# Optimization experiments

Measured on AMD Instinct MI355X. Metric: run time of the kernel, lower is better.

## Reference

```python
import jax, jax.numpy as jnp
import numpy as np

EPS = 1e-5  # torch BatchNorm1d default eps


def _bn(x, p):
    # eval-mode batchnorm; p = stacked [gamma, beta, running_mean, running_var], shape [4, C]
    g, b, m, v = p
    return (x - m[:, None]) * jax.lax.rsqrt(v[:, None] + EPS) * g[:, None] + b[:, None]


def _conv(w, x):
    # 1x1 Conv1d == channel matmul: w [O,C], x [B,C,N] -> [B,O,N]
    return jnp.einsum('oc,bcn->bon', w, x)


def _sa(x, qk_w, v_w, v_b, t_w, t_b, bnp):
    # offset self-attention; q_conv.weight is tied to k_conv.weight in the original
    q = jnp.einsum('oc,bcn->bno', qk_w, x)          # [B,N,C/4]
    k = _conv(qk_w, x)                              # [B,C/4,N]
    v = _conv(v_w, x) + v_b[None, :, None]          # [B,C,N]
    attn = jax.nn.softmax(jnp.einsum('bno,bom->bnm', q, k), axis=-1)  # [B,N,N]
    attn = attn / (1e-9 + attn.sum(axis=1, keepdims=True))            # L1 re-norm over dim 1
    x_r = jnp.einsum('bcn,bnm->bcm', v, attn)       # [B,C,N]
    x_r = jax.nn.relu(_bn(_conv(t_w, x - x_r) + t_b[None, :, None], bnp))
    return x + x_r


def setup_inputs():
    key = jax.random.key(0)
    ks = iter(jax.random.split(key, 64))
    def n(shape, s=0.1):
        return jax.random.normal(next(ks), shape, jnp.float32) * s
    def bn_p(c):
        g = jax.random.uniform(next(ks), (c,), jnp.float32, 0.5, 1.5)
        b = n((c,))
        m = n((c,))
        v = jax.random.uniform(next(ks), (c,), jnp.float32, 0.5, 1.5)
        return jnp.stack([g, b, m, v])
    B, C, N = 16, 16, 2048
    return {
        'x': jax.random.normal(next(ks), (B, C, N), jnp.float32),
        'conv1_w': n((128, 16)), 'bn1': bn_p(128),
        'conv2_w': n((16, 128)), 'bn2': bn_p(16),
        'sa_qk_w': n((4, 4, 16)), 'sa_v_w': n((4, 16, 16)), 'sa_v_b': n((4, 16)),
        'sa_trans_w': n((4, 16, 16)), 'sa_trans_b': n((4, 16)),
        'sa_bn': jnp.stack([bn_p(16) for _ in range(4)]),
        'fuse_w': n((128, 64)), 'fuse_bn': bn_p(128),
        'convs1_w': n((512, 264)), 'convs1_b': n((512,)), 'bns1': bn_p(512),
        'convs2_w': n((256, 512)), 'convs2_b': n((256,)), 'bns2': bn_p(256),
        'convs3_w': n((16, 256)), 'convs3_b': n((16,)),
    }


def reference(x, conv1_w, bn1, conv2_w, bn2, sa_qk_w, sa_v_w, sa_v_b,
              sa_trans_w, sa_trans_b, sa_bn, fuse_w, fuse_bn,
              convs1_w, convs1_b, bns1, convs2_w, convs2_b, bns2,
              convs3_w, convs3_b):
    B, _, N = x.shape
    h = jax.nn.relu(_bn(_conv(conv1_w, x), bn1))   # [B,128,N]
    h = jax.nn.relu(_bn(_conv(conv2_w, h), bn2))   # [B,16,N]
    feats = []
    for i in range(4):
        h = _sa(h, sa_qk_w[i], sa_v_w[i], sa_v_b[i], sa_trans_w[i], sa_trans_b[i], sa_bn[i])
        feats.append(h)
    xqq = jnp.concatenate(feats, axis=1)           # [B,64,N]
    xqqw = jax.nn.leaky_relu(_bn(_conv(fuse_w, xqq), fuse_bn), 0.2)  # [B,128,N]
    # faithful to original (including the [1]-indexing quirk):
    x_max = jnp.argmax(xqqw, axis=2)               # [B,128] argmax indices (torch.max(...)[1])
    x_avg = jnp.mean(xqqw, axis=2)[1]              # [128] batch element 1's channel means
    x_max_f = jnp.broadcast_to(x_max.astype(jnp.float32)[:, :, None], (B, 128, N))
    x_avg_f = jnp.broadcast_to(x_avg.reshape(B, -1)[:, :, None], (B, 128 // B, N))
    g = jnp.concatenate([xqqw, x_max_f, x_avg_f], axis=1)  # [B,264,N]
    g = jax.nn.relu(_bn(_conv(convs1_w, g) + convs1_b[None, :, None], bns1))
    # dropout is identity in eval mode
    g = jax.nn.relu(_bn(_conv(convs2_w, g) + convs2_b[None, :, None], bns2))
    return _conv(convs3_w, g) + convs3_b[None, :, None]  # [B,16,N]
```

## Files before the change

### kernel.cpp

```cpp
#include <hip/hip_runtime.h>
#include <stdint.h>

typedef __bf16 bf16_t;
typedef __bf16 bf16x8 __attribute__((ext_vector_type(8)));
typedef __bf16 bf16x4 __attribute__((ext_vector_type(4)));
typedef float f32x4 __attribute__((ext_vector_type(4)));
typedef float f32x2 __attribute__((ext_vector_type(2)));

#define LOG2E 1.4426950408889634f

__device__ __forceinline__ float relu_(float v) { return v > 0.f ? v : 0.f; }

__global__ __launch_bounds__(256) void k_prep(
    const float* __restrict__ convs1_w, const float* __restrict__ convs2_w,
    const float* __restrict__ bn1, const float* __restrict__ bn2,
    const float* __restrict__ sa_bn, const float* __restrict__ sa_trans_b,
    const float* __restrict__ fuse_bn, const float* __restrict__ convs1_b,
    const float* __restrict__ bns1, const float* __restrict__ convs2_b,
    const float* __restrict__ bns2,
    bf16_t* __restrict__ wbuf1, bf16_t* __restrict__ wbuf2, float* __restrict__ params)
{
  int idx = blockIdx.x * 256 + threadIdx.x;
  for (int it = 0; it < 3; ++it) {
    int i = idx + it * 65536;
    if (i < 65536) {
      int o = i >> 7, c = i & 127;
      wbuf1[i] = (bf16_t)convs1_w[o * 264 + c];
    } else if (i < 65536 + 131072) {
      int j = i - 65536;
      wbuf2[j] = (bf16_t)convs2_w[j];
    }
  }
  if (blockIdx.x == 0) {
    for (int t = threadIdx.x; t < 1104; t += 256) {
      float g, be, m, v, extra = 0.f; int so, ho;
      if (t < 128)      { g=bn1[t]; be=bn1[128+t]; m=bn1[256+t]; v=bn1[384+t]; so=t; ho=128+t; }
      else if (t < 144) { int u=t-128; g=bn2[u]; be=bn2[16+u]; m=bn2[32+u]; v=bn2[48+u]; so=256+u; ho=272+u; }
      else if (t < 208) { int u=t-144; int L=u>>4, o=u&15; const float* p=sa_bn+L*64;
                          g=p[o]; be=p[16+o]; m=p[32+o]; v=p[48+o];
                          extra=sa_trans_b[L*16+o]; so=288+u; ho=352+u; }
      else if (t < 336) { int u=t-208; g=fuse_bn[u]; be=fuse_bn[128+u]; m=fuse_bn[256+u]; v=fuse_bn[384+u]; so=416+u; ho=544+u; }
      else if (t < 848) { int u=t-336; g=bns1[u]; be=bns1[512+u]; m=bns1[1024+u]; v=bns1[1536+u]; extra=convs1_b[u]; so=672+u; ho=1184+u; }
      else              { int u=t-848; g=bns2[u]; be=bns2[256+u]; m=bns2[512+u]; v=bns2[768+u]; extra=convs2_b[u]; so=1696+u; ho=1952+u; }
      float sc = g * rsqrtf(v + 1e-5f);
      params[so] = sc;
      params[ho] = (extra - m) * sc + be;
    }
  }
}

__global__ __launch_bounds__(256) void k_convs(const float* __restrict__ x,
    const float* __restrict__ w1, const float* __restrict__ w2,
    const float* __restrict__ params, const float* __restrict__ qk_w,
    const float* __restrict__ v_w, const float* __restrict__ v_b,
    float* __restrict__ h0, float* __restrict__ kbuf, float* __restrict__ vbufT)
{
  __shared__ float xs[16 * 64];
  __shared__ float ws1[128 * 17];
  __shared__ float ws2[16 * 129];
  __shared__ __align__(16) float h1s[128 * 64];
  __shared__ float hcv[64 * 17];
  __shared__ float qk[64], vw[256], vb[16], sc1[128], sh1[128], sc2[16], sh2[16];
  int t = threadIdx.x;
  int bid = blockIdx.x;
  int b = bid >> 5, n0 = (bid & 31) * 64;
  for (int i = t; i < 1024; i += 256) { int c = i >> 6, col = i & 63; xs[i] = x[((size_t)b * 16 + c) * 2048 + n0 + col]; }
  for (int i = t; i < 2048; i += 256) { int o = i >> 4, c = i & 15;  ws1[o * 17 + c]  = w1[i]; }
  for (int i = t; i < 2048; i += 256) { int o = i >> 7, c = i & 127; ws2[o * 129 + c] = w2[i]; }
  if (t < 64) qk[t] = qk_w[t];
  vw[t] = v_w[t];
  if (t < 16) { vb[t] = v_b[t]; sc2[t] = params[256 + t]; sh2[t] = params[272 + t]; }
  if (t < 128) { sc1[t] = params[t]; sh1[t] = params[128 + t]; }
  __syncthreads();
  int col = t & 63, og = t >> 6;
  float xr[16];
#pragma unroll
  for (int c = 0; c < 16; ++c) xr[c] = xs[c * 64 + col];
#pragma unroll 4
  for (int i = 0; i < 32; ++i) {
    int o = og * 32 + i;
    float s = 0.f;
#pragma unroll
    for (int c = 0; c < 16; ++c) s = fmaf(ws1[o * 17 + c], xr[c], s);
    h1s[o * 64 + col] = relu_(fmaf(s, sc1[o], sh1[o]));
  }
  __syncthreads();
  float a[4] = {0.f, 0.f, 0.f, 0.f};
  for (int c = 0; c < 128; ++c) {
    float hv = h1s[c * 64 + col];
#pragma unroll
    for (int oo = 0; oo < 4; ++oo) a[oo] = fmaf(ws2[(og * 4 + oo) * 129 + c], hv, a[oo]);
  }
#pragma unroll
  for (int oo = 0; oo < 4; ++oo) {
    int o = og * 4 + oo;
    float v = relu_(fmaf(a[oo], sc2[o], sh2[o]));
    h0[((size_t)b * 16 + o) * 2048 + n0 + col] = v;
    hcv[col * 17 + o] = v;
  }
  __syncthreads();
  float hr[16];
#pragma unroll
  for (int c = 0; c < 16; ++c) hr[c] = hcv[col * 17 + c];
#pragma unroll
  for (int i = 0; i < 5; ++i) {
    int u = og * 5 + i;
    const float* W = (u < 4) ? &qk[u * 16] : &vw[(u - 4) * 16];
    float s = (u < 4) ? 0.f : vb[u - 4];
#pragma unroll
    for (int c = 0; c < 16; ++c) s = fmaf(W[c], hr[c], s);
    if (u < 4) kbuf[((size_t)b * 2048 + n0 + col) * 4 + u] = s;
    else       vbufT[((size_t)b * 2048 + n0 + col) * 16 + (u - 4)] = s;
  }
}

__global__ __launch_bounds__(256) void k_rowstats(const float* __restrict__ kbuf, float* __restrict__ Lpart)
{
  __shared__ float4 kch[128];
  int bid = blockIdx.x;
  int b = bid >> 7, nt = (bid >> 4) & 7, ms = bid & 15;
  int t = threadIdx.x;
  const float4* kb = (const float4*)kbuf + b * 2048;
  if (t < 128) kch[t] = kb[ms * 128 + t];
  __syncthreads();
  int n = nt * 256 + t;
  float4 q = kb[n];
  q.x *= LOG2E; q.y *= LOG2E; q.z *= LOG2E; q.w *= LOG2E;
  float L = 0.f;
#pragma unroll 4
  for (int m = 0; m < 128; ++m) {
    float4 k4 = kch[m];
    float s = fmaf(q.x, k4.x, fmaf(q.y, k4.y, fmaf(q.z, k4.z, q.w * k4.w)));
    L += exp2f(s);
  }
  Lpart[((size_t)ms * 16 + b) * 2048 + n] = L;
}

__global__ __launch_bounds__(256) void k_colaccum(const float* __restrict__ kbuf, const float* __restrict__ vbufT,
    const float* __restrict__ Lpart, float* __restrict__ parts)
{
  __shared__ __align__(16) float ku[128 * 8];
  __shared__ __align__(16) float vch[128 * 16];
  int bid = blockIdx.x;
  int b = bid >> 6, mt = (bid >> 4) & 3, ns = bid & 15;
  int t = threadIdx.x;
  if (t < 128) {
    int n = ns * 128 + t;
    float4 k4 = ((const float4*)kbuf)[b * 2048 + n];
    float Ls = 0.f;
#pragma unroll
    for (int s = 0; s < 16; ++s) Ls += Lpart[((size_t)s * 16 + b) * 2048 + n];
    *(float4*)&ku[t * 8] = k4;
    ku[t * 8 + 4] = -__log2f(Ls);
  } else {
    int s = t - 128;
    int n = ns * 128 + s;
    const float4* vp = (const float4*)&vbufT[((size_t)b * 2048 + n) * 16];
    *(float4*)&vch[s * 16 + 0]  = vp[0];
    *(float4*)&vch[s * 16 + 4]  = vp[1];
    *(float4*)&vch[s * 16 + 8]  = vp[2];
    *(float4*)&vch[s * 16 + 12] = vp[3];
  }
  __syncthreads();
  int m0 = mt * 512 + t;
  float4 qa = ((const float4*)kbuf)[b * 2048 + m0];
  float4 qb = ((const float4*)kbuf)[b * 2048 + m0 + 256];
  qa.x *= LOG2E; qa.y *= LOG2E; qa.z *= LOG2E; qa.w *= LOG2E;
  qb.x *= LOG2E; qb.y *= LOG2E; qb.z *= LOG2E; qb.w *= LOG2E;
  f32x2 acc0[8], acc1[8];
#pragma unroll
  for (int j = 0; j < 8; ++j) { acc0[j] = (f32x2){0.f, 0.f}; acc1[j] = (f32x2){0.f, 0.f}; }
  float den0 = 0.f, den1 = 0.f;
#pragma unroll 2
  for (int nn = 0; nn < 128; ++nn) {
    f32x4 k4 = *(const f32x4*)&ku[nn * 8];
    float lg = ku[nn * 8 + 4];
    float s0 = fmaf(qa.x, k4[0], fmaf(qa.y, k4[1], fmaf(qa.z, k4[2], fmaf(qa.w, k4[3], lg))));
    float s1 = fmaf(qb.x, k4[0], fmaf(qb.y, k4[1], fmaf(qb.z, k4[2], fmaf(qb.w, k4[3], lg))));
    float e0 = exp2f(s0), e1 = exp2f(s1);
    den0 += e0; den1 += e1;
    f32x4 va = *(const f32x4*)&vch[nn * 16 + 0];
    f32x4 vbb = *(const f32x4*)&vch[nn * 16 + 4];
    f32x4 vc = *(const f32x4*)&vch[nn * 16 + 8];
    f32x4 vd = *(const f32x4*)&vch[nn * 16 + 12];
    f32x2 ev0 = {e0, e0}, ev1 = {e1, e1};
    f32x2 p0 = {va[0], va[1]},  p1 = {va[2], va[3]};
    f32x2 p2 = {vbb[0], vbb[1]}, p3 = {vbb[2], vbb[3]};
    f32x2 p4 = {vc[0], vc[1]},  p5 = {vc[2], vc[3]};
    f32x2 p6 = {vd[0], vd[1]},  p7 = {vd[2], vd[3]};
    acc0[0] += ev0 * p0; acc0[1] += ev0 * p1; acc0[2] += ev0 * p2; acc0[3] += ev0 * p3;
    acc0[4] += ev0 * p4; acc0[5] += ev0 * p5; acc0[6] += ev0 * p6; acc0[7] += ev0 * p7;
    acc1[0] += ev1 * p0; acc1[1] += ev1 * p1; acc1[2] += ev1 * p2; acc1[3] += ev1 * p3;
    acc1[4] += ev1 * p4; acc1[5] += ev1 * p5; acc1[6] += ev1 * p6; acc1[7] += ev1 * p7;
  }
  float* p = parts + ((size_t)(ns * 16 + b) * 17) * 2048 + m0;
#pragma unroll
  for (int c = 0; c < 16; ++c) p[(size_t)c * 2048] = acc0[c >> 1][c & 1];
  p[(size_t)16 * 2048] = den0;
  p += 256;
#pragma unroll
  for (int c = 0; c < 16; ++c) p[(size_t)c * 2048] = acc1[c >> 1][c & 1];
  p[(size_t)16 * 2048] = den1;
}

__global__ __launch_bounds__(256) void k_epilogue(const float* __restrict__ parts,
    const float* __restrict__ hin, int hbs, const float* __restrict__ t_w,
    const float* __restrict__ params, int layer, float* __restrict__ hout,
    const float* __restrict__ qk_w, const float* __restrict__ v_w, const float* __restrict__ v_b,
    float* __restrict__ kbuf, float* __restrict__ vbufT)
{
  __shared__ __align__(16) float pd[17 * 64];
  __shared__ float hs[16 * 64];
  __shared__ float dl[16 * 64];
  __shared__ float hv[64 * 17];
  __shared__ float tw[256], qk[64], vw[256], vb[16], sc[16], sh[16];
  int t = threadIdx.x;
  int bid = blockIdx.x;
  int b = bid >> 5, n0 = (bid & 31) * 64;
  tw[t] = t_w[t];
  if (qk_w) { if (t < 64) qk[t] = qk_w[t]; vw[t] = v_w[t]; if (t < 16) vb[t] = v_b[t]; }
  if (t < 16) { sc[t] = params[288 + layer * 16 + t]; sh[t] = params[352 + layer * 16 + t]; }
  for (int i = t; i < 272; i += 256) {
    int r = i >> 4, c4 = (i & 15) << 2;
    f32x4 s = {0.f, 0.f, 0.f, 0.f};
#pragma unroll
    for (int sp = 0; sp < 16; ++sp)
      s += *(const f32x4*)&parts[((size_t)(sp * 16 + b) * 17 + r) * 2048 + n0 + c4];
    *(f32x4*)&pd[r * 64 + c4] = s;
  }
  for (int i = t; i < 1024; i += 256) {
    int c = i >> 6, col = i & 63;
    hs[i] = hin[(size_t)b * hbs + (size_t)c * 2048 + n0 + col];
  }
  __syncthreads();
  int col = t & 63, g4 = t >> 6;
  float inv = 1.f / (1e-9f + pd[16 * 64 + col]);
#pragma unroll
  for (int j = 0; j < 4; ++j) {
    int c = g4 * 4 + j;
    dl[c * 64 + col] = hs[c * 64 + col] - pd[c * 64 + col] * inv;
  }
  __syncthreads();
#pragma unroll
  for (int j = 0; j < 4; ++j) {
    int o = g4 * 4 + j;
    float y = 0.f;
#pragma unroll
    for (int c = 0; c < 16; ++c) y = fmaf(tw[o * 16 + c], dl[c * 64 + col], y);
    y = relu_(fmaf(y, sc[o], sh[o]));
    float hh = hs[o * 64 + col] + y;
    hout[(size_t)b * 64 * 2048 + (size_t)o * 2048 + n0 + col] = hh;
    hv[col * 17 + o] = hh;
  }
  if (qk_w) {
    __syncthreads();
    float hr[16];
#pragma unroll
    for (int c = 0; c < 16; ++c) hr[c] = hv[col * 17 + c];
#pragma unroll
    for (int i = 0; i < 5; ++i) {
      int u = g4 * 5 + i;
      const float* W = (u < 4) ? &qk[u * 16] : &vw[(u - 4) * 16];
      float s = (u < 4) ? 0.f : vb[u - 4];
#pragma unroll
      for (int c = 0; c < 16; ++c) s = fmaf(W[c], hr[c], s);
      if (u < 4) kbuf[((size_t)b * 2048 + n0 + col) * 4 + u] = s;
      else       vbufT[((size_t)b * 2048 + n0 + col) * 16 + (u - 4)] = s;
    }
  }
}

__global__ __launch_bounds__(256) void k_fuse(const float* __restrict__ feats, const float* __restrict__ fw,
    const float* __restrict__ params, float* __restrict__ xqqw, bf16_t* __restrict__ gbuf)
{
  __shared__ float ws[128 * 65];
  __shared__ __align__(16) float fst[64 * 64];
  __shared__ float sc[128], sh[128];
  int t = threadIdx.x, bid = blockIdx.x;
  int b = bid >> 5, n0 = (bid & 31) * 64;
  for (int i = t; i < 8192; i += 256) { int o = i >> 6, c = i & 63; ws[o * 65 + c] = fw[i]; }
  for (int i = t; i < 4096; i += 256) { int c = i >> 6, col = i & 63; fst[i] = feats[((size_t)b * 64 + c) * 2048 + n0 + col]; }
  if (t < 128) { sc[t] = params[416 + t]; sh[t] = params[544 + t]; }
  __syncthreads();
  int cg = t & 7, og = t >> 3;
  f32x2 acc[4][4];
#pragma unroll
  for (int oo = 0; oo < 4; ++oo)
#pragma unroll
    for (int j = 0; j < 4; ++j) acc[oo][j] = (f32x2){0.f, 0.f};
  for (int c = 0; c < 64; ++c) {
    const f32x2* fp = (const f32x2*)&fst[c * 64 + cg * 8];
    f32x2 f0 = fp[0], f1 = fp[1], f2v = fp[2], f3 = fp[3];
#pragma unroll
    for (int oo = 0; oo < 4; ++oo) {
      float w = ws[(og * 4 + oo) * 65 + c];
      f32x2 wv = {w, w};
      acc[oo][0] += wv * f0; acc[oo][1] += wv * f1;
      acc[oo][2] += wv * f2v; acc[oo][3] += wv * f3;
    }
  }
  float y[4][8];
#pragma unroll
  for (int oo = 0; oo < 4; ++oo) {
    int o = og * 4 + oo;
    float s0 = sc[o], s1 = sh[o];
#pragma unroll
    for (int j = 0; j < 8; ++j) {
      float v = fmaf(acc[oo][j >> 1][j & 1], s0, s1);
      y[oo][j] = v > 0.f ? v : 0.2f * v;
    }
    float4 v0 = {y[oo][0], y[oo][1], y[oo][2], y[oo][3]};
    float4 v1 = {y[oo][4], y[oo][5], y[oo][6], y[oo][7]};
    *(float4*)&xqqw[((size_t)b * 128 + o) * 2048 + n0 + cg * 8] = v0;
    *(float4*)&xqqw[((size_t)b * 128 + o) * 2048 + n0 + cg * 8 + 4] = v1;
  }
#pragma unroll
  for (int j = 0; j < 8; ++j) {
    int col = n0 + cg * 8 + j;
    bf16x4 pk;
    pk[0] = (bf16_t)y[0][j]; pk[1] = (bf16_t)y[1][j];
    pk[2] = (bf16_t)y[2][j]; pk[3] = (bf16_t)y[3][j];
    *(bf16x4*)&gbuf[((size_t)b * 2048 + col) * 128 + og * 4] = pk;
  }
}

__global__ __launch_bounds__(256) void k_argmax(const float* __restrict__ xqqw,
    float* __restrict__ xmaxf, float* __restrict__ xavg)
{
  __shared__ float sv[256]; __shared__ int si[256]; __shared__ float ss[256];
  int bo = blockIdx.x;
  int b = bo >> 7, o = bo & 127;
  const float* row = xqqw + (size_t)bo * 2048;
  int tid = threadIdx.x;
  float best = -3.4e38f; int bi = 0; float sum = 0.f;
#pragma unroll
  for (int j = 0; j < 8; ++j) {
    int n = j * 256 + tid;
    float v = row[n];
    sum += v;
    if (v > best) { best = v; bi = n; }
  }
  sv[tid] = best; si[tid] = bi; ss[tid] = sum;
  __syncthreads();
  for (int s = 128; s > 0; s >>= 1) {
    if (tid < s) {
      float v2 = sv[tid + s]; int i2 = si[tid + s];
      if (v2 > sv[tid] || (v2 == sv[tid] && i2 < si[tid])) { sv[tid] = v2; si[tid] = i2; }
      ss[tid] += ss[tid + s];
    }
    __syncthreads();
  }
  if (tid == 0) {
    xmaxf[bo] = (float)si[0];
    if (b == 1) xavg[o] = ss[0] * (1.0f / 2048.0f);
  }
}

__global__ __launch_bounds__(256) void k_bias2(const float* __restrict__ w1,
    const float* __restrict__ xmaxf, const float* __restrict__ xavg,
    const float* __restrict__ params, float* __restrict__ bias2)
{
  int id = blockIdx.x * 256 + threadIdx.x;
  int o = id >> 4, b = id & 15;
  const float* wr = w1 + (size_t)o * 264;
  float s = 0.f;
  for (int u = 0; u < 128; ++u) s = fmaf(wr[128 + u], xmaxf[b * 128 + u], s);
#pragma unroll
  for (int u = 0; u < 8; ++u)  s = fmaf(wr[256 + u], xavg[b * 8 + u], s);
  bias2[b * 512 + o] = s * params[672 + o];
}

__global__ __launch_bounds__(256) void k_gemm(const bf16_t* __restrict__ A, const bf16_t* __restrict__ Bm,
    const float* __restrict__ scp, const float* __restrict__ shp, const float* __restrict__ bias2,
    bf16_t* __restrict__ Cout, int M, int K, int mtiles)
{
  __shared__ bf16_t At[128 * 32];
  __shared__ bf16_t Bt[128 * 32];
  int tid = threadIdx.x;
  int mt = blockIdx.x % mtiles, ct = blockIdx.x / mtiles;
  int srow = tid >> 2, scol = (tid & 3) << 3;
  const bf16_t* ga = A  + (size_t)(mt * 128 + srow) * K + scol;
  const bf16_t* gb = Bm + (size_t)(ct * 128 + srow) * K + scol;
  int lane = tid & 63, wave = tid >> 6;
  int wr = (wave >> 1) * 64, wc = (wave & 1) * 64;
  int frow = lane & 15, fk = (lane >> 4) * 8;
  const f32x4 z4 = {0.f, 0.f, 0.f, 0.f};
  f32x4 acc[4][4];
#pragma unroll
  for (int i = 0; i < 4; ++i)
#pragma unroll
    for (int j = 0; j < 4; ++j) acc[i][j] = z4;
  uint4 ra0 = *(const uint4*)ga, ra1 = *(const uint4*)(ga + (size_t)64 * K);
  uint4 rb0 = *(const uint4*)gb, rb1 = *(const uint4*)(gb + (size_t)64 * K);
  int ksteps = K >> 5;
  for (int ks = 0; ks < ksteps; ++ks) {
    __syncthreads();
    *(uint4*)&At[tid * 8] = ra0;  *(uint4*)&At[2048 + tid * 8] = ra1;
    *(uint4*)&Bt[tid * 8] = rb0;  *(uint4*)&Bt[2048 + tid * 8] = rb1;
    __syncthreads();
    if (ks + 1 < ksteps) {
      ra0 = *(const uint4*)(ga + (ks + 1) * 32);
      ra1 = *(const uint4*)(ga + (size_t)64 * K + (ks + 1) * 32);
      rb0 = *(const uint4*)(gb + (ks + 1) * 32);
      rb1 = *(const uint4*)(gb + (size_t)64 * K + (ks + 1) * 32);
    }
    bf16x8 af[4], bfr[4];
#pragma unroll
    for (int i = 0; i < 4; ++i) af[i]  = *(const bf16x8*)&At[(wr + i * 16 + frow) * 32 + fk];
#pragma unroll
    for (int j = 0; j < 4; ++j) bfr[j] = *(const bf16x8*)&Bt[(wc + j * 16 + frow) * 32 + fk];
#pragma unroll
    for (int i = 0; i < 4; ++i)
#pragma unroll
      for (int j = 0; j < 4; ++j)
        acc[i][j] = __builtin_amdgcn_mfma_f32_16x16x32_bf16(af[i], bfr[j], acc[i][j], 0, 0, 0);
  }
  int crow = (lane >> 4) * 4, ccol = lane & 15;
#pragma unroll
  for (int i = 0; i < 4; ++i) {
    int o0 = mt * 128 + wr + i * 16 + crow;
    float s0 = scp[o0], s1 = scp[o0+1], s2 = scp[o0+2], s3 = scp[o0+3];
    float t0 = shp[o0], t1 = shp[o0+1], t2 = shp[o0+2], t3 = shp[o0+3];
#pragma unroll
    for (int j = 0; j < 4; ++j) {
      int bn = ct * 128 + wc + j * 16 + ccol;
      float b0 = 0.f, b1 = 0.f, b2 = 0.f, b3 = 0.f;
      if (bias2) {
        const float* bp = bias2 + (size_t)(bn >> 11) * M + o0;
        b0 = bp[0]; b1 = bp[1]; b2 = bp[2]; b3 = bp[3];
      }
      bf16x4 pk;
      pk[0] = (bf16_t)relu_(fmaf(acc[i][j][0], s0, t0 + b0));
      pk[1] = (bf16_t)relu_(fmaf(acc[i][j][1], s1, t1 + b1));
      pk[2] = (bf16_t)relu_(fmaf(acc[i][j][2], s2, t2 + b2));
      pk[3] = (bf16_t)relu_(fmaf(acc[i][j][3], s3, t3 + b3));
      *(bf16x4*)(Cout + (size_t)bn * M + o0) = pk;
    }
  }
}

__global__ __launch_bounds__(256) void k_gemm3(const bf16_t* __restrict__ g2, const float* __restrict__ w3,
    const float* __restrict__ b3, float* __restrict__ out)
{
  __shared__ float wsT[4096];
  __shared__ float bb[16];
  int t = threadIdx.x;
  for (int i = t; i < 4096; i += 256) { int o = i >> 8, k = i & 255; wsT[k * 16 + o] = w3[i]; }
  if (t < 16) bb[t] = b3[t];
  __syncthreads();
  int col = blockIdx.x * 64 + (t & 63);
  int og = t >> 6;
  int b = col >> 11, n = col & 2047;
  const bf16_t* g = g2 + (size_t)col * 256;
  float acc[4] = {0.f, 0.f, 0.f, 0.f};
  for (int k0 = 0; k0 < 256; k0 += 8) {
    bf16x8 gv8 = *(const bf16x8*)(g + k0);
#pragma unroll
    for (int kk = 0; kk < 8; ++kk) {
      float gv = (float)gv8[kk];
      const float* wr = &wsT[(k0 + kk) * 16 + og * 4];
#pragma unroll
      for (int oo = 0; oo < 4; ++oo) acc[oo] = fmaf(wr[oo], gv, acc[oo]);
    }
  }
  float* op = out + (size_t)b * 16 * 2048 + n;
#pragma unroll
  for (int oo = 0; oo < 4; ++oo) {
    int o = og * 4 + oo;
    op[(size_t)o * 2048] = acc[oo] + bb[o];
  }
}

extern "C" void kernel_launch(void* const* d_in, const int* in_sizes, int n_in,
                              void* d_out, int out_size, void* d_ws, size_t ws_size,
                              hipStream_t stream)
{
  const float* x         = (const float*)d_in[0];
  const float* conv1_w   = (const float*)d_in[1];
  const float* bn1       = (const float*)d_in[2];
  const float* conv2_w   = (const float*)d_in[3];
  const float* bn2       = (const float*)d_in[4];
  const float* sa_qk_w   = (const float*)d_in[5];
  const float* sa_v_w    = (const float*)d_in[6];
  const float* sa_v_b    = (const float*)d_in[7];
  const float* sa_trans_w= (const float*)d_in[8];
  const float* sa_trans_b= (const float*)d_in[9];
  const float* sa_bn     = (const float*)d_in[10];
  const float* fuse_w    = (const float*)d_in[11];
  const float* fuse_bn   = (const float*)d_in[12];
  const float* convs1_w  = (const float*)d_in[13];
  const float* convs1_b  = (const float*)d_in[14];
  const float* bns1      = (const float*)d_in[15];
  const float* convs2_w  = (const float*)d_in[16];
  const float* convs2_b  = (const float*)d_in[17];
  const float* bns2      = (const float*)d_in[18];
  const float* convs3_w  = (const float*)d_in[19];
  const float* convs3_b  = (const float*)d_in[20];

  char* ws = (char*)d_ws;
  float*  xqqw  = (float*)(ws + 0);
  float*  feats = (float*)(ws + 16777216);
  float*  h0    = (float*)(ws + 25165824);
  float*  kbuf  = (float*)(ws + 27262976);
  float*  vbufT = (float*)(ws + 27787264);
  float*  Lpart = (float*)(ws + 29884416);
  float*  parts = (float*)(ws + 31981568);
  bf16_t* g1    = (bf16_t*)(ws + 0);
  bf16_t* g2    = (bf16_t*)(ws + 33554432);
  bf16_t* gbuf  = (bf16_t*)(ws + 50331648);
  bf16_t* wbuf1 = (bf16_t*)(ws + 67633152);
  bf16_t* wbuf2 = (bf16_t*)(ws + 67764224);
  float*  params= (float*)(ws + 68026368);
  float*  xmaxf = (float*)(ws + 68042752);
  float*  xavg  = (float*)(ws + 68050944);
  float*  bias2 = (float*)(ws + 68055040);

  k_prep<<<256, 256, 0, stream>>>(convs1_w, convs2_w, bn1, bn2, sa_bn, sa_trans_b, fuse_bn,
                                  convs1_b, bns1, convs2_b, bns2, wbuf1, wbuf2, params);
  k_convs<<<512, 256, 0, stream>>>(x, conv1_w, conv2_w, params, sa_qk_w, sa_v_w, sa_v_b,
                                   h0, kbuf, vbufT);
  for (int i = 0; i < 4; ++i) {
    k_rowstats<<<2048, 256, 0, stream>>>(kbuf, Lpart);
    k_colaccum<<<1024, 256, 0, stream>>>(kbuf, vbufT, Lpart, parts);
    const float* hin = (i == 0) ? h0 : (feats + (size_t)(i - 1) * 16 * 2048);
    int hbs = (i == 0) ? 16 * 2048 : 64 * 2048;
    bool last = (i == 3);
    k_epilogue<<<512, 256, 0, stream>>>(parts, hin, hbs, sa_trans_w + i * 256, params, i,
        feats + (size_t)i * 16 * 2048,
        last ? nullptr : sa_qk_w + (i + 1) * 64,
        last ? nullptr : sa_v_w + (i + 1) * 256,
        last ? nullptr : sa_v_b + (i + 1) * 16,
        kbuf, vbufT);
  }
  k_fuse<<<512, 256, 0, stream>>>(feats, fuse_w, params, xqqw, gbuf);
  k_argmax<<<2048, 256, 0, stream>>>(xqqw, xmaxf, xavg);
  k_bias2<<<32, 256, 0, stream>>>(convs1_w, xmaxf, xavg, params, bias2);
  k_gemm<<<1024, 256, 0, stream>>>(wbuf1, gbuf, params + 672, params + 1184, bias2, g1, 512, 128, 4);
  k_gemm<<<512, 256, 0, stream>>>(wbuf2, g1, params + 1696, params + 1952, nullptr, g2, 256, 512, 2);
  k_gemm3<<<512, 256, 0, stream>>>(g2, convs3_w, convs3_b, (float*)d_out);
}
```

Before: 518.3 us.

## Move attention column accumulation to bf16 MFMA with split-precision and atomic row sums

The scalar FMA loop that accumulated exp-weighted V columns and denominators is replaced by a kernel that issues 16x16x32 bf16 MFMA instructions. Both V and the exponentials are split into hi/lo bf16 parts so the products keep close to fp32 accuracy, and a ones-vector MFMA produces the column sums. Row-stat partial sums are now combined with atomicAdd into a per-layer buffer that the prep kernel zeroes, which removes the 16-way partial read in the consumer. The cost is three MFMAs per product plus extra conversion work, and atomic float adds make the summation order nondeterministic.

```diff
diff --git a/kernel.cpp b/kernel.cpp
--- a/kernel.cpp
+++ b/kernel.cpp
@@ -18,9 +18,12 @@
     const float* __restrict__ fuse_bn, const float* __restrict__ convs1_b,
     const float* __restrict__ bns1, const float* __restrict__ convs2_b,
     const float* __restrict__ bns2,
-    bf16_t* __restrict__ wbuf1, bf16_t* __restrict__ wbuf2, float* __restrict__ params)
+    bf16_t* __restrict__ wbuf1, bf16_t* __restrict__ wbuf2, float* __restrict__ params,
+    float* __restrict__ Lbuf)
 {
   int idx = blockIdx.x * 256 + threadIdx.x;
+  Lbuf[idx] = 0.f;
+  Lbuf[idx + 65536] = 0.f;
   for (int it = 0; it < 3; ++it) {
     int i = idx + it * 65536;
     if (i < 65536) {
@@ -114,7 +117,7 @@
   }
 }
 
-__global__ __launch_bounds__(256) void k_rowstats(const float* __restrict__ kbuf, float* __restrict__ Lpart)
+__global__ __launch_bounds__(256) void k_rowstats(const float* __restrict__ kbuf, float* __restrict__ Lb)
 {
   __shared__ float4 kch[128];
   int bid = blockIdx.x;
@@ -133,74 +136,80 @@
     float s = fmaf(q.x, k4.x, fmaf(q.y, k4.y, fmaf(q.z, k4.z, q.w * k4.w)));
     L += exp2f(s);
   }
-  Lpart[((size_t)ms * 16 + b) * 2048 + n] = L;
-}
-
-__global__ __launch_bounds__(256) void k_colaccum(const float* __restrict__ kbuf, const float* __restrict__ vbufT,
-    const float* __restrict__ Lpart, float* __restrict__ parts)
-{
-  __shared__ __align__(16) float ku[128 * 8];
-  __shared__ __align__(16) float vch[128 * 16];
+  atomicAdd(&Lb[b * 2048 + n], L);
+}
+
+__global__ __launch_bounds__(256, 4) void k_attn(const float* __restrict__ kbuf,
+    const float* __restrict__ vbufT, const float* __restrict__ Lb, float* __restrict__ parts)
+{
+  __shared__ float skn[128 * 8];
+  __shared__ __align__(16) float4 skm[512];
+  int t = threadIdx.x;
   int bid = blockIdx.x;
-  int b = bid >> 6, mt = (bid >> 4) & 3, ns = bid & 15;
-  int t = threadIdx.x;
+  int b = bid >> 6, ns = (bid >> 2) & 15, mq = bid & 3;
   if (t < 128) {
     int n = ns * 128 + t;
     float4 k4 = ((const float4*)kbuf)[b * 2048 + n];
-    float Ls = 0.f;
-#pragma unroll
-    for (int s = 0; s < 16; ++s) Ls += Lpart[((size_t)s * 16 + b) * 2048 + n];
-    *(float4*)&ku[t * 8] = k4;
-    ku[t * 8 + 4] = -__log2f(Ls);
-  } else {
-    int s = t - 128;
-    int n = ns * 128 + s;
-    const float4* vp = (const float4*)&vbufT[((size_t)b * 2048 + n) * 16];
-    *(float4*)&vch[s * 16 + 0]  = vp[0];
-    *(float4*)&vch[s * 16 + 4]  = vp[1];
-    *(float4*)&vch[s * 16 + 8]  = vp[2];
-    *(float4*)&vch[s * 16 + 12] = vp[3];
-  }
-  __syncthreads();
-  int m0 = mt * 512 + t;
-  float4 qa = ((const float4*)kbuf)[b * 2048 + m0];
-  float4 qb = ((const float4*)kbuf)[b * 2048 + m0 + 256];
-  qa.x *= LOG2E; qa.y *= LOG2E; qa.z *= LOG2E; qa.w *= LOG2E;
-  qb.x *= LOG2E; qb.y *= LOG2E; qb.z *= LOG2E; qb.w *= LOG2E;
-  f32x2 acc0[8], acc1[8];
-#pragma unroll
-  for (int j = 0; j < 8; ++j) { acc0[j] = (f32x2){0.f, 0.f}; acc1[j] = (f32x2){0.f, 0.f}; }
-  float den0 = 0.f, den1 = 0.f;
-#pragma unroll 2
-  for (int nn = 0; nn < 128; ++nn) {
-    f32x4 k4 = *(const f32x4*)&ku[nn * 8];
-    float lg = ku[nn * 8 + 4];
-    float s0 = fmaf(qa.x, k4[0], fmaf(qa.y, k4[1], fmaf(qa.z, k4[2], fmaf(qa.w, k4[3], lg))));
-    float s1 = fmaf(qb.x, k4[0], fmaf(qb.y, k4[1], fmaf(qb.z, k4[2], fmaf(qb.w, k4[3], lg))));
-    float e0 = exp2f(s0), e1 = exp2f(s1);
-    den0 += e0; den1 += e1;
-    f32x4 va = *(const f32x4*)&vch[nn * 16 + 0];
-    f32x4 vbb = *(const f32x4*)&vch[nn * 16 + 4];
-    f32x4 vc = *(const f32x4*)&vch[nn * 16 + 8];
-    f32x4 vd = *(const f32x4*)&vch[nn * 16 + 12];
-    f32x2 ev0 = {e0, e0}, ev1 = {e1, e1};
-    f32x2 p0 = {va[0], va[1]},  p1 = {va[2], va[3]};
-    f32x2 p2 = {vbb[0], vbb[1]}, p3 = {vbb[2], vbb[3]};
-    f32x2 p4 = {vc[0], vc[1]},  p5 = {vc[2], vc[3]};
-    f32x2 p6 = {vd[0], vd[1]},  p7 = {vd[2], vd[3]};
-    acc0[0] += ev0 * p0; acc0[1] += ev0 * p1; acc0[2] += ev0 * p2; acc0[3] += ev0 * p3;
-    acc0[4] += ev0 * p4; acc0[5] += ev0 * p5; acc0[6] += ev0 * p6; acc0[7] += ev0 * p7;
-    acc1[0] += ev1 * p0; acc1[1] += ev1 * p1; acc1[2] += ev1 * p2; acc1[3] += ev1 * p3;
-    acc1[4] += ev1 * p4; acc1[5] += ev1 * p5; acc1[6] += ev1 * p6; acc1[7] += ev1 * p7;
-  }
-  float* p = parts + ((size_t)(ns * 16 + b) * 17) * 2048 + m0;
-#pragma unroll
-  for (int c = 0; c < 16; ++c) p[(size_t)c * 2048] = acc0[c >> 1][c & 1];
-  p[(size_t)16 * 2048] = den0;
-  p += 256;
-#pragma unroll
-  for (int c = 0; c < 16; ++c) p[(size_t)c * 2048] = acc1[c >> 1][c & 1];
-  p[(size_t)16 * 2048] = den1;
+    *(float4*)&skn[t * 8] = k4;
+    skn[t * 8 + 4] = -__log2f(Lb[b * 2048 + n]);
+  }
+  skm[t]       = ((const float4*)kbuf)[b * 2048 + mq * 512 + t];
+  skm[t + 256] = ((const float4*)kbuf)[b * 2048 + mq * 512 + t + 256];
+  __syncthreads();
+  int lane = t & 63, w = t >> 6;
+  int lg16 = lane >> 4, c = lane & 15;
+  bf16x8 vhi[4], vlo[4];
+#pragma unroll
+  for (int s = 0; s < 4; ++s) {
+#pragma unroll
+    for (int j = 0; j < 8; ++j) {
+      int n = ns * 128 + s * 32 + lg16 * 8 + j;
+      float v = vbufT[((size_t)b * 2048 + n) * 16 + c];
+      bf16_t h = (bf16_t)v;
+      vhi[s][j] = h;
+      vlo[s][j] = (bf16_t)(v - (float)h);
+    }
+  }
+  bf16x8 ones;
+#pragma unroll
+  for (int j = 0; j < 8; ++j) ones[j] = (bf16_t)1.0f;
+
+  float* pb = parts + ((size_t)(ns * 16 + b) * 17) * 2048;
+  for (int it = 0; it < 8; ++it) {
+    int tm = w * 8 + it;
+    int mb = mq * 512 + tm * 16;
+    float4 km = skm[tm * 16 + c];
+    km.x *= LOG2E; km.y *= LOG2E; km.z *= LOG2E; km.w *= LOG2E;
+    f32x4 acc = {0.f, 0.f, 0.f, 0.f};
+    f32x4 acc2 = {0.f, 0.f, 0.f, 0.f};
+#pragma unroll
+    for (int s = 0; s < 4; ++s) {
+      float e[8];
+#pragma unroll
+      for (int j = 0; j < 8; ++j) {
+        const float* kp = &skn[(s * 32 + lg16 * 8 + j) * 8];
+        float sc = fmaf(km.x, kp[0], fmaf(km.y, kp[1], fmaf(km.z, kp[2], fmaf(km.w, kp[3], kp[4]))));
+        e[j] = exp2f(sc);
+      }
+      bf16x8 eh, el;
+#pragma unroll
+      for (int j = 0; j < 8; ++j) {
+        bf16_t h = (bf16_t)e[j];
+        eh[j] = h;
+        el[j] = (bf16_t)(e[j] - (float)h);
+      }
+      acc  = __builtin_amdgcn_mfma_f32_16x16x32_bf16(vhi[s], eh, acc, 0, 0, 0);
+      acc  = __builtin_amdgcn_mfma_f32_16x16x32_bf16(vlo[s], eh, acc, 0, 0, 0);
+      acc  = __builtin_amdgcn_mfma_f32_16x16x32_bf16(vhi[s], el, acc, 0, 0, 0);
+      acc2 = __builtin_amdgcn_mfma_f32_16x16x32_bf16(ones,  eh, acc2, 0, 0, 0);
+      acc2 = __builtin_amdgcn_mfma_f32_16x16x32_bf16(ones,  el, acc2, 0, 0, 0);
+    }
+    float* pp = pb + mb + c;
+#pragma unroll
+    for (int r = 0; r < 4; ++r)
+      pp[(size_t)(lg16 * 4 + r) * 2048] = acc[r];
+    if (lane < 16) pp[(size_t)16 * 2048] = acc2[0];
+  }
 }
 
 __global__ __launch_bounds__(256) void k_epilogue(const float* __restrict__ parts,
@@ -503,7 +512,7 @@
   float*  h0    = (float*)(ws + 25165824);
   float*  kbuf  = (float*)(ws + 27262976);
   float*  vbufT = (float*)(ws + 27787264);
-  float*  Lpart = (float*)(ws + 29884416);
+  float*  Lbuf  = (float*)(ws + 29884416);
   float*  parts = (float*)(ws + 31981568);
   bf16_t* g1    = (bf16_t*)(ws + 0);
   bf16_t* g2    = (bf16_t*)(ws + 33554432);
@@ -516,12 +525,13 @@
   float*  bias2 = (float*)(ws + 68055040);
 
   k_prep<<<256, 256, 0, stream>>>(convs1_w, convs2_w, bn1, bn2, sa_bn, sa_trans_b, fuse_bn,
-                                  convs1_b, bns1, convs2_b, bns2, wbuf1, wbuf2, params);
+                                  convs1_b, bns1, convs2_b, bns2, wbuf1, wbuf2, params, Lbuf);
   k_convs<<<512, 256, 0, stream>>>(x, conv1_w, conv2_w, params, sa_qk_w, sa_v_w, sa_v_b,
                                    h0, kbuf, vbufT);
   for (int i = 0; i < 4; ++i) {
-    k_rowstats<<<2048, 256, 0, stream>>>(kbuf, Lpart);
-    k_colaccum<<<1024, 256, 0, stream>>>(kbuf, vbufT, Lpart, parts);
+    float* Lb = Lbuf + (size_t)i * 32768;
+    k_rowstats<<<2048, 256, 0, stream>>>(kbuf, Lb);
+    k_attn<<<1024, 256, 0, stream>>>(kbuf, vbufT, Lb, parts);
     const float* hin = (i == 0) ? h0 : (feats + (size_t)(i - 1) * 16 * 2048);
     int hbs = (i == 0) ? 16 * 2048 : 64 * 2048;
     bool last = (i == 3);
```

Result: slower. 914.0 us (+76.3%).
